# Kernel tuning notes

Measured on AMD Instinct MI355X. Metric: run time of the kernel, lower is better.

Reference implementation:

```python
import jax, jax.numpy as jnp
import numpy as np

D_MODEL = 1024
NUM_HEADS = 16
THETA = 10000.0


def _trunc_normal(key, shape):
    # matches torch.nn.init.trunc_normal_(std=std, a=-3*std, b=3*std)
    std = (2.0 / (shape[0] + shape[1])) ** 0.5
    return jax.random.truncated_normal(key, -3.0, 3.0, shape, dtype=jnp.float32) * std


def setup_inputs() -> dict:
    key = jax.random.key(0)
    kx, kq, kk, kv, ko = jax.random.split(key, 5)
    B, S, D = 2, 2048, D_MODEL
    return {
        "x": jax.random.normal(kx, (B, S, D), dtype=jnp.float32),
        "Wq": _trunc_normal(kq, (D, D)),  # torch Linear weight: [out, in]
        "Wk": _trunc_normal(kk, (D, D)),
        "Wv": _trunc_normal(kv, (D, D)),
        "Wo": _trunc_normal(ko, (D, D)),
        "token_positions": jnp.arange(S, dtype=jnp.int32),
    }


def _rope(x, token_positions):
    # x: [B, H, S, d_k]; RoPE on interleaved pairs (k r) with r=2
    d_k = x.shape[-1]
    inv_freq = THETA ** (-2.0 * jnp.arange(d_k // 2, dtype=jnp.float32) / d_k)
    ang = token_positions.astype(jnp.float32)[:, None] * inv_freq[None, :]  # [S, d_k/2]
    sin, cos = jnp.sin(ang).astype(x.dtype), jnp.cos(ang).astype(x.dtype)
    x0, x1 = x[..., 0::2], x[..., 1::2]
    y0 = x0 * cos - x1 * sin
    y1 = x0 * sin + x1 * cos
    return jnp.stack([y0, y1], axis=-1).reshape(x.shape)


def reference(x, Wq, Wk, Wv, Wo, token_positions):
    B, S, D = x.shape
    H = NUM_HEADS
    d_k = D // H

    def proj(W):  # y = x @ W^T, split heads -> [B, H, S, d_k]
        y = jnp.einsum('bsd,ed->bse', x, W)
        return y.reshape(B, S, H, d_k).transpose(0, 2, 1, 3)

    q = _rope(proj(Wq), token_positions)
    k = _rope(proj(Wk), token_positions)
    v = proj(Wv)

    # causal mask: attend where pos_k <= pos_q
    mask = token_positions[None, :] <= token_positions[:, None]  # [S_q, S_k]
    logits = jnp.einsum('bhqd,bhkd->bhqk', q, k) / (d_k ** 0.5)
    logits = jnp.where(mask, logits, -jnp.inf)
    scores = jax.nn.softmax(logits, axis=-1)
    attn = jnp.einsum('bhqk,bhkd->bhqd', scores, v)  # [B, H, S, d_k]
    attn = attn.transpose(0, 2, 1, 3).reshape(B, S, D)
    return jnp.einsum('bsd,ed->bse', attn, Wo)
```

## Files before the change

### kernel.cpp

```cpp
#include <hip/hip_runtime.h>
#include <hip/hip_bf16.h>

typedef __attribute__((ext_vector_type(8))) short s16x8;
typedef __attribute__((ext_vector_type(4))) float f32x4;

__device__ __forceinline__ unsigned short f2b(float x) {
  unsigned int u = __float_as_uint(x);
  u = (u + 0x7fffu + ((u >> 16) & 1u)) >> 16;
  return (unsigned short)u;
}

__device__ __forceinline__ unsigned int pkbf(float a, float b) {
  return (unsigned int)f2b(a) | ((unsigned int)f2b(b) << 16);
}

__device__ __forceinline__ float b2f(unsigned short u) {
  return __uint_as_float((unsigned int)u << 16);
}

__device__ __forceinline__ void gl2lds16(const unsigned short* g, unsigned short* lds) {
  __builtin_amdgcn_global_load_lds(
      (const __attribute__((address_space(1))) unsigned int*)g,
      (__attribute__((address_space(3))) unsigned int*)lds, 16, 0, 0);
}

__global__ __launch_bounds__(256) void cast_all(
    const float* __restrict__ x,  const float* __restrict__ Wq,
    const float* __restrict__ Wk, const float* __restrict__ Wv,
    const float* __restrict__ Wo, unsigned short* __restrict__ dst) {
  int i = blockIdx.x * 256 + threadIdx.x;
  const float* src;
  int off;
  if (i < 1048576) { src = x; off = i; }
  else {
    int j = i - 1048576;
    int seg = j >> 18;
    off = j & 262143;
    src = (seg == 0) ? Wq : (seg == 1) ? Wk : (seg == 2) ? Wv : Wo;
  }
  const float4 v = ((const float4*)src)[off];
  ushort4 o;
  o.x = f2b(v.x); o.y = f2b(v.y); o.z = f2b(v.z); o.w = f2b(v.w);
  ((ushort4*)dst)[i] = o;
}

#define KDIM 1024

__global__ __launch_bounds__(256, 4) void gemm_qkv(
    const unsigned short* __restrict__ A,
    const unsigned short* __restrict__ Bt,
    const int* __restrict__ tok,
    unsigned short* __restrict__ Qo,
    unsigned short* __restrict__ Ko,
    unsigned short* __restrict__ Vt) {
  __shared__ unsigned short As[2][128 * 32];
  __shared__ unsigned short Bs[2][128 * 32];
  const int tid = threadIdx.x;
  const int bid = blockIdx.x;
  const int xcd = bid & 7;
  const int loc = bid >> 3;
  const int m0 = (loc / 3) * 128;
  const int n0 = (xcd * 3 + loc % 3) * 128;
  const int w = tid >> 6, lane = tid & 63;
  const int ln = lane & 15, quad = lane >> 4;
  const int wm = (w >> 1) * 64, wn = (w & 1) * 64;

  const int rr = lane >> 2;
  const int gsw = ((lane & 3) ^ ((rr ^ (rr >> 2)) & 3)) * 8;
  const int sr = (ln ^ (ln >> 2)) & 3;

  const f32x4 zero = {0.f, 0.f, 0.f, 0.f};
  f32x4 acc[4][4];
#pragma unroll
  for (int i = 0; i < 4; ++i)
#pragma unroll
    for (int j = 0; j < 4; ++j) acc[i][j] = zero;

#define QKV_STAGE(kb, p)                                                              \
  do {                                                                                \
    int col = (kb) * 32 + gsw;                                                        \
    gl2lds16(A  + (size_t)(m0 + w * 32 + rr) * KDIM + col,      &As[p][(w * 32) * 32]);      \
    gl2lds16(A  + (size_t)(m0 + w * 32 + 16 + rr) * KDIM + col, &As[p][(w * 32 + 16) * 32]); \
    gl2lds16(Bt + (size_t)(n0 + w * 32 + rr) * KDIM + col,      &Bs[p][(w * 32) * 32]);      \
    gl2lds16(Bt + (size_t)(n0 + w * 32 + 16 + rr) * KDIM + col, &Bs[p][(w * 32 + 16) * 32]); \
  } while (0)

  QKV_STAGE(0, 0);
  for (int kb = 0; kb < 32; ++kb) {
    const int p = kb & 1;
    __syncthreads();
    if (kb < 31) QKV_STAGE(kb + 1, p ^ 1);
    s16x8 af[4], bfr[4];
#pragma unroll
    for (int i = 0; i < 4; ++i)
      af[i] = *(const s16x8*)(&As[p][(wm + i * 16 + ln) * 32 + ((quad ^ sr) * 8)]);
#pragma unroll
    for (int j = 0; j < 4; ++j)
      bfr[j] = *(const s16x8*)(&Bs[p][(wn + j * 16 + ln) * 32 + ((quad ^ sr) * 8)]);
#pragma unroll
    for (int i = 0; i < 4; ++i)
#pragma unroll
      for (int j = 0; j < 4; ++j)
        acc[i][j] = __builtin_amdgcn_mfma_f32_16x16x32_bf16(af[i], bfr[j], acc[i][j], 0, 0, 0);
  }
#undef QKV_STAGE

#pragma unroll
  for (int j = 0; j < 4; ++j) {
    int gn = n0 + wn + j * 16 + ln;
    bool isV = (gn >= 2048);
    int e = isV ? (gn - 2048) : (gn & 1023);
    int h = e >> 6, d = e & 63;
    float inv = __expf(-0.2878231366f * (float)(d >> 1));
#pragma unroll
    for (int i = 0; i < 4; ++i) {
      int gmb = m0 + wm + i * 16 + quad * 4;
#pragma unroll
      for (int r = 0; r < 4; ++r) {
        float val = acc[i][j][r];
        float part = __shfl_xor(val, 1, 64);
        int m = gmb + r;
        int b = m >> 11, s = m & 2047;
        if (!isV) {
          float pos = (float)tok[s];
          float ang = pos * inv;
          float sn, cs;
          __sincosf(ang, &sn, &cs);
          float x0 = (d & 1) ? part : val;
          float x1 = (d & 1) ? val : part;
          float y = (d & 1) ? (x0 * sn + x1 * cs) : (x0 * cs - x1 * sn);
          unsigned short* dst = (gn < 1024) ? Qo : Ko;
          dst[(((size_t)b * 16 + h) * 2048 + s) * 64 + d] = f2b(y);
        } else {
          Vt[(((size_t)b * 16 + h) * 64 + d) * 2048 + s] = f2b(val);
        }
      }
    }
  }
}

__global__ __launch_bounds__(256, 3) void attn_partial(
    const unsigned short* __restrict__ Q,
    const unsigned short* __restrict__ K,
    const unsigned short* __restrict__ Vt,
    unsigned short* __restrict__ Opart,
    float2* __restrict__ ML) {
  __shared__ unsigned short Ks[64 * 64];
  __shared__ unsigned short Vs[64 * 64];
  __shared__ unsigned short Pt[4][16 * 72];

  const int bid = blockIdx.x;
  const int xcd = bid & 7;
  const int loc = bid >> 3;
  const int bh = xcd * 4 + (loc & 3);
  const int widx = loc >> 2;
  int c, qh;
  if (widx < 28) {
    if (widx < 13)      { c = 0; qh = 3 + widx; }
    else if (widx < 22) { c = 1; qh = 7 + (widx - 13); }
    else if (widx < 27) { c = 2; qh = 11 + (widx - 22); }
    else                { c = 3; qh = 15; }
  } else {
    int s = widx - 28;
    int wt = s >> 2;
    c = s & 3;
    qh = 4 * c + 2 - wt;
  }
  const int kbeg = c * 512;
  const int khi = min(kbeg + 512, qh * 128 + 128);

  const int tid = threadIdx.x;
  const int w = tid >> 6, lane = tid & 63;
  const int ln = lane & 15, quad = lane >> 4;
  const int qb = qh * 128 + w * 32;

  const unsigned short* Qb = Q + (size_t)bh * 2048 * 64;
  const unsigned short* Kb = K + (size_t)bh * 2048 * 64;
  const unsigned short* Vb = Vt + (size_t)bh * 64 * 2048;

  const int srow = w * 16 + (lane >> 3);
  const int sg = (lane & 7) ^ (srow & 7);

  s16x8 bq[2][2];
#pragma unroll
  for (int u = 0; u < 2; ++u)
#pragma unroll
    for (int hh = 0; hh < 2; ++hh)
      bq[u][hh] = *(const s16x8*)(&Qb[(size_t)(qb + u * 16 + ln) * 64 + hh * 32 + quad * 8]);

  const f32x4 zero = {0.f, 0.f, 0.f, 0.f};
  f32x4 o[2][4];
#pragma unroll
  for (int u = 0; u < 2; ++u)
#pragma unroll
    for (int j = 0; j < 4; ++j) o[u][j] = zero;
  float m_i[2] = {-3e38f, -3e38f};
  float l_i[2] = {0.f, 0.f};

  const int rdsw = ((ln & 7) * 8);

  for (int k0 = kbeg; k0 < khi; k0 += 64) {
    __syncthreads();
    gl2lds16(Kb + (size_t)(k0 + srow) * 64 + sg * 8,       &Ks[(w * 16) * 64]);
    gl2lds16(Kb + (size_t)(k0 + srow + 8) * 64 + sg * 8,   &Ks[(w * 16 + 8) * 64]);
    gl2lds16(Vb + (size_t)srow * 2048 + k0 + sg * 8,       &Vs[(w * 16) * 64]);
    gl2lds16(Vb + (size_t)(srow + 8) * 2048 + k0 + sg * 8, &Vs[(w * 16 + 8) * 64]);
    __syncthreads();

    s16x8 ka[4][2];
#pragma unroll
    for (int t = 0; t < 4; ++t)
#pragma unroll
      for (int hh = 0; hh < 2; ++hh)
        ka[t][hh] = *(const s16x8*)(&Ks[(t * 16 + ln) * 64 + (((hh * 4 + quad) * 8) ^ rdsw)]);

#pragma unroll
    for (int u = 0; u < 2; ++u) {
      const int q = qb + u * 16 + ln;
      f32x4 st[4];
#pragma unroll
      for (int t = 0; t < 4; ++t) {
        f32x4 s = __builtin_amdgcn_mfma_f32_16x16x32_bf16(ka[t][0], bq[u][0], zero, 0, 0, 0);
        st[t] = __builtin_amdgcn_mfma_f32_16x16x32_bf16(ka[t][1], bq[u][1], s, 0, 0, 0);
      }
      float lm = -3e38f;
#pragma unroll
      for (int t = 0; t < 4; ++t)
#pragma unroll
        for (int r = 0; r < 4; ++r) {
          int kk = k0 + t * 16 + quad * 4 + r;
          float v = st[t][r] * 0.125f;
          v = (kk > q) ? -3e38f : v;
          st[t][r] = v;
          lm = fmaxf(lm, v);
        }
      lm = fmaxf(lm, __shfl_xor(lm, 16, 64));
      lm = fmaxf(lm, __shfl_xor(lm, 32, 64));
      float mn = fmaxf(m_i[u], lm);
      float al = __expf(m_i[u] - mn);
      float rs = 0.f;
#pragma unroll
      for (int t = 0; t < 4; ++t)
#pragma unroll
        for (int r = 0; r < 4; ++r) {
          float p = __expf(st[t][r] - mn);
          st[t][r] = p;
          rs += p;
        }
      rs += __shfl_xor(rs, 16, 64);
      rs += __shfl_xor(rs, 32, 64);
      m_i[u] = mn;
      l_i[u] = l_i[u] * al + rs;
#pragma unroll
      for (int j = 0; j < 4; ++j) o[u][j] *= al;

#pragma unroll
      for (int t = 0; t < 4; ++t) {
        uint2 pv;
        pv.x = pkbf(st[t][0], st[t][1]);
        pv.y = pkbf(st[t][2], st[t][3]);
        *(uint2*)(&Pt[w][ln * 72 + t * 16 + quad * 4]) = pv;
      }
      __builtin_amdgcn_wave_barrier();
#pragma unroll
      for (int hh = 0; hh < 2; ++hh) {
        s16x8 pb = *(const s16x8*)(&Pt[w][ln * 72 + hh * 32 + quad * 8]);
#pragma unroll
        for (int j = 0; j < 4; ++j) {
          s16x8 va = *(const s16x8*)(&Vs[(j * 16 + ln) * 64 + (((hh * 4 + quad) * 8) ^ rdsw)]);
          o[u][j] = __builtin_amdgcn_mfma_f32_16x16x32_bf16(va, pb, o[u][j], 0, 0, 0);
        }
      }
      __builtin_amdgcn_wave_barrier();
    }
  }

#pragma unroll
  for (int u = 0; u < 2; ++u) {
    int s = qb + u * 16 + ln;
    size_t row = ((size_t)bh * 4 + c) * 2048 + s;
    if (quad == 0) ML[row] = make_float2(m_i[u], l_i[u]);
    size_t base = row * 64;
#pragma unroll
    for (int j = 0; j < 4; ++j) {
      ushort4 o4;
      o4.x = f2b(o[u][j][0]);
      o4.y = f2b(o[u][j][1]);
      o4.z = f2b(o[u][j][2]);
      o4.w = f2b(o[u][j][3]);
      *(ushort4*)(&Opart[base + j * 16 + quad * 4]) = o4;
    }
  }
}

__global__ __launch_bounds__(256) void attn_merge(
    const unsigned short* __restrict__ Opart,
    const float2* __restrict__ ML,
    unsigned short* __restrict__ Ao) {
  int idx = blockIdx.x * 256 + threadIdx.x;
  int d0 = (idx & 7) * 8;
  int q  = (idx >> 3) & 2047;
  int bh = idx >> 14;
  int nc = (q >> 9) + 1;

  float m_c[4], l_c[4];
  float M = -3e38f;
  for (int c = 0; c < nc; ++c) {
    float2 ml = ML[((size_t)bh * 4 + c) * 2048 + q];
    m_c[c] = ml.x; l_c[c] = ml.y;
    M = fmaxf(M, ml.x);
  }
  float acc[8] = {0, 0, 0, 0, 0, 0, 0, 0};
  float L = 0.f;
  for (int c = 0; c < nc; ++c) {
    float wc = __expf(m_c[c] - M);
    L += wc * l_c[c];
    const ushort4* p = (const ushort4*)(Opart + (((size_t)bh * 4 + c) * 2048 + q) * 64 + d0);
    ushort4 a = p[0], bvec = p[1];
    acc[0] += wc * b2f(a.x); acc[1] += wc * b2f(a.y);
    acc[2] += wc * b2f(a.z); acc[3] += wc * b2f(a.w);
    acc[4] += wc * b2f(bvec.x); acc[5] += wc * b2f(bvec.y);
    acc[6] += wc * b2f(bvec.z); acc[7] += wc * b2f(bvec.w);
  }
  float invL = 1.0f / L;
  int b = bh >> 4, h = bh & 15;
  unsigned short* dst = Ao + ((size_t)b * 2048 + q) * 1024 + h * 64 + d0;
  ushort4 o0, o1;
  o0.x = f2b(acc[0] * invL); o0.y = f2b(acc[1] * invL);
  o0.z = f2b(acc[2] * invL); o0.w = f2b(acc[3] * invL);
  o1.x = f2b(acc[4] * invL); o1.y = f2b(acc[5] * invL);
  o1.z = f2b(acc[6] * invL); o1.w = f2b(acc[7] * invL);
  ((ushort4*)dst)[0] = o0;
  ((ushort4*)dst)[1] = o1;
}

__global__ __launch_bounds__(256, 3) void gemm_out(
    const unsigned short* __restrict__ A,
    const unsigned short* __restrict__ Bt,
    float* __restrict__ out) {
  __shared__ unsigned short As[2][128 * 32];
  __shared__ unsigned short Bs[2][128 * 32];
  const int tid = threadIdx.x;
  const int bid = blockIdx.x;
  const int m0 = (bid >> 3) * 128;
  const int n0 = (bid & 7) * 128;
  const int w = tid >> 6, lane = tid & 63;
  const int ln = lane & 15, quad = lane >> 4;
  const int wm = (w >> 1) * 64, wn = (w & 1) * 64;

  const int rr = lane >> 2;
  const int gsw = ((lane & 3) ^ ((rr ^ (rr >> 2)) & 3)) * 8;
  const int sr = (ln ^ (ln >> 2)) & 3;

  const f32x4 zero = {0.f, 0.f, 0.f, 0.f};
  f32x4 acc[4][4];
#pragma unroll
  for (int i = 0; i < 4; ++i)
#pragma unroll
    for (int j = 0; j < 4; ++j) acc[i][j] = zero;

#define OUT_STAGE(kb, p)                                                              \
  do {                                                                                \
    int col = (kb) * 32 + gsw;                                                        \
    gl2lds16(A  + (size_t)(m0 + w * 32 + rr) * KDIM + col,      &As[p][(w * 32) * 32]);      \
    gl2lds16(A  + (size_t)(m0 + w * 32 + 16 + rr) * KDIM + col, &As[p][(w * 32 + 16) * 32]); \
    gl2lds16(Bt + (size_t)(n0 + w * 32 + rr) * KDIM + col,      &Bs[p][(w * 32) * 32]);      \
    gl2lds16(Bt + (size_t)(n0 + w * 32 + 16 + rr) * KDIM + col, &Bs[p][(w * 32 + 16) * 32]); \
  } while (0)

  OUT_STAGE(0, 0);
  for (int kb = 0; kb < 32; ++kb) {
    const int p = kb & 1;
    __syncthreads();
    if (kb < 31) OUT_STAGE(kb + 1, p ^ 1);
    s16x8 af[4], bfr[4];
#pragma unroll
    for (int i = 0; i < 4; ++i)
      af[i] = *(const s16x8*)(&As[p][(wm + i * 16 + ln) * 32 + ((quad ^ sr) * 8)]);
#pragma unroll
    for (int j = 0; j < 4; ++j)
      bfr[j] = *(const s16x8*)(&Bs[p][(wn + j * 16 + ln) * 32 + ((quad ^ sr) * 8)]);
#pragma unroll
    for (int i = 0; i < 4; ++i)
#pragma unroll
      for (int j = 0; j < 4; ++j)
        acc[i][j] = __builtin_amdgcn_mfma_f32_16x16x32_bf16(af[i], bfr[j], acc[i][j], 0, 0, 0);
  }
#undef OUT_STAGE

#pragma unroll
  for (int i = 0; i < 4; ++i) {
    int gmb = m0 + wm + i * 16 + quad * 4;
#pragma unroll
    for (int j = 0; j < 4; ++j) {
      int gn = n0 + wn + j * 16 + ln;
#pragma unroll
      for (int r = 0; r < 4; ++r)
        out[(size_t)(gmb + r) * 1024 + gn] = acc[i][j][r];
    }
  }
}

extern "C" void kernel_launch(void* const* d_in, const int* in_sizes, int n_in,
                              void* d_out, int out_size, void* d_ws, size_t ws_size,
                              hipStream_t stream) {
  const float* x  = (const float*)d_in[0];
  const float* Wq = (const float*)d_in[1];
  const float* Wk = (const float*)d_in[2];
  const float* Wv = (const float*)d_in[3];
  const float* Wo = (const float*)d_in[4];
  const int* tok  = (const int*)d_in[5];
  float* out = (float*)d_out;

  char* ws = (char*)d_ws;
  unsigned short* xb    = (unsigned short*)(ws);
  unsigned short* Wcat  = (unsigned short*)(ws + (8ull  << 20));
  unsigned short* Wob   = (unsigned short*)(ws + (14ull << 20));
  unsigned short* Qb    = (unsigned short*)(ws + (16ull << 20));
  unsigned short* Kb    = (unsigned short*)(ws + (24ull << 20));
  unsigned short* Vtb   = (unsigned short*)(ws + (32ull << 20));
  unsigned short* Ab    = (unsigned short*)(ws + (40ull << 20));
  unsigned short* Opart = (unsigned short*)(ws + (48ull << 20));
  float2*         ML    = (float2*)        (ws + (80ull << 20));

  cast_all<<<dim3(8192), dim3(256), 0, stream>>>(x, Wq, Wk, Wv, Wo, xb);
  gemm_qkv<<<dim3(768), dim3(256), 0, stream>>>(xb, Wcat, tok, Qb, Kb, Vtb);
  attn_partial<<<dim3(1280), dim3(256), 0, stream>>>(Qb, Kb, Vtb, Opart, ML);
  attn_merge<<<dim3(2048), dim3(256), 0, stream>>>(Opart, ML, Ab);
  gemm_out<<<dim3(256), dim3(256), 0, stream>>>(Ab, Wob, out);
}
```

Before: 212.3 us.

## Double-buffer attention K/V tiles; single-buffer output GEMM with wider K tile

The attention partial kernel now double-buffers its K and V shared-memory tiles and prefetches the next 64-key tile while computing on the current one, dropping one barrier per iteration. The output projection GEMM moves the other way: it drops its double buffer for a single 128x64 buffer per operand, loads synchronously with two barriers, and uses an 8-way XOR swizzle. The GEMM change halves the number of K iterations but loses load/compute overlap. The attention change doubles K/V shared memory, which may limit occupancy.

```diff
diff --git a/kernel.cpp b/kernel.cpp
--- a/kernel.cpp
+++ b/kernel.cpp
@@ -145,8 +145,8 @@
     const unsigned short* __restrict__ Vt,
     unsigned short* __restrict__ Opart,
     float2* __restrict__ ML) {
-  __shared__ unsigned short Ks[64 * 64];
-  __shared__ unsigned short Vs[64 * 64];
+  __shared__ unsigned short Ks[2][64 * 64];
+  __shared__ unsigned short Vs[2][64 * 64];
   __shared__ unsigned short Pt[4][16 * 72];
 
   const int bid = blockIdx.x;
@@ -168,6 +168,7 @@
   }
   const int kbeg = c * 512;
   const int khi = min(kbeg + 512, qh * 128 + 128);
+  const int nit = (khi - kbeg) >> 6;
 
   const int tid = threadIdx.x;
   const int w = tid >> 6, lane = tid & 63;
@@ -181,6 +182,14 @@
   const int srow = w * 16 + (lane >> 3);
   const int sg = (lane & 7) ^ (srow & 7);
 
+#define ATTN_STAGE(k0, p)                                                            \
+  do {                                                                               \
+    gl2lds16(Kb + (size_t)((k0) + srow) * 64 + sg * 8,       &Ks[p][(w * 16) * 64]);      \
+    gl2lds16(Kb + (size_t)((k0) + srow + 8) * 64 + sg * 8,   &Ks[p][(w * 16 + 8) * 64]);  \
+    gl2lds16(Vb + (size_t)srow * 2048 + (k0) + sg * 8,       &Vs[p][(w * 16) * 64]);      \
+    gl2lds16(Vb + (size_t)(srow + 8) * 2048 + (k0) + sg * 8, &Vs[p][(w * 16 + 8) * 64]);  \
+  } while (0)
+
   s16x8 bq[2][2];
 #pragma unroll
   for (int u = 0; u < 2; ++u)
@@ -199,20 +208,19 @@
 
   const int rdsw = ((ln & 7) * 8);
 
-  for (int k0 = kbeg; k0 < khi; k0 += 64) {
+  ATTN_STAGE(kbeg, 0);
+  for (int it = 0; it < nit; ++it) {
+    const int p = it & 1;
+    const int k0 = kbeg + it * 64;
     __syncthreads();
-    gl2lds16(Kb + (size_t)(k0 + srow) * 64 + sg * 8,       &Ks[(w * 16) * 64]);
-    gl2lds16(Kb + (size_t)(k0 + srow + 8) * 64 + sg * 8,   &Ks[(w * 16 + 8) * 64]);
-    gl2lds16(Vb + (size_t)srow * 2048 + k0 + sg * 8,       &Vs[(w * 16) * 64]);
-    gl2lds16(Vb + (size_t)(srow + 8) * 2048 + k0 + sg * 8, &Vs[(w * 16 + 8) * 64]);
-    __syncthreads();
+    if (it + 1 < nit) ATTN_STAGE(k0 + 64, p ^ 1);
 
     s16x8 ka[4][2];
 #pragma unroll
     for (int t = 0; t < 4; ++t)
 #pragma unroll
       for (int hh = 0; hh < 2; ++hh)
-        ka[t][hh] = *(const s16x8*)(&Ks[(t * 16 + ln) * 64 + (((hh * 4 + quad) * 8) ^ rdsw)]);
+        ka[t][hh] = *(const s16x8*)(&Ks[p][(t * 16 + ln) * 64 + (((hh * 4 + quad) * 8) ^ rdsw)]);
 
 #pragma unroll
     for (int u = 0; u < 2; ++u) {
@@ -243,9 +251,9 @@
       for (int t = 0; t < 4; ++t)
 #pragma unroll
         for (int r = 0; r < 4; ++r) {
-          float p = __expf(st[t][r] - mn);
-          st[t][r] = p;
-          rs += p;
+          float pv = __expf(st[t][r] - mn);
+          st[t][r] = pv;
+          rs += pv;
         }
       rs += __shfl_xor(rs, 16, 64);
       rs += __shfl_xor(rs, 32, 64);
@@ -267,13 +275,14 @@
         s16x8 pb = *(const s16x8*)(&Pt[w][ln * 72 + hh * 32 + quad * 8]);
 #pragma unroll
         for (int j = 0; j < 4; ++j) {
-          s16x8 va = *(const s16x8*)(&Vs[(j * 16 + ln) * 64 + (((hh * 4 + quad) * 8) ^ rdsw)]);
+          s16x8 va = *(const s16x8*)(&Vs[p][(j * 16 + ln) * 64 + (((hh * 4 + quad) * 8) ^ rdsw)]);
           o[u][j] = __builtin_amdgcn_mfma_f32_16x16x32_bf16(va, pb, o[u][j], 0, 0, 0);
         }
       }
       __builtin_amdgcn_wave_barrier();
     }
   }
+#undef ATTN_STAGE
 
 #pragma unroll
   for (int u = 0; u < 2; ++u) {
@@ -338,8 +347,8 @@
     const unsigned short* __restrict__ A,
     const unsigned short* __restrict__ Bt,
     float* __restrict__ out) {
-  __shared__ unsigned short As[2][128 * 32];
-  __shared__ unsigned short Bs[2][128 * 32];
+  __shared__ unsigned short As[128 * 64];
+  __shared__ unsigned short Bs[128 * 64];
   const int tid = threadIdx.x;
   const int bid = blockIdx.x;
   const int m0 = (bid >> 3) * 128;
@@ -348,9 +357,9 @@
   const int ln = lane & 15, quad = lane >> 4;
   const int wm = (w >> 1) * 64, wn = (w & 1) * 64;
 
-  const int rr = lane >> 2;
-  const int gsw = ((lane & 3) ^ ((rr ^ (rr >> 2)) & 3)) * 8;
-  const int sr = (ln ^ (ln >> 2)) & 3;
+  const int srow = w * 32 + (lane >> 3);
+  const int sg = (lane & 7) ^ (lane >> 3);
+  const int rs = ln & 7;
 
   const f32x4 zero = {0.f, 0.f, 0.f, 0.f};
   f32x4 acc[4][4];
@@ -359,35 +368,30 @@
 #pragma unroll
     for (int j = 0; j < 4; ++j) acc[i][j] = zero;
 
-#define OUT_STAGE(kb, p)                                                              \
-  do {                                                                                \
-    int col = (kb) * 32 + gsw;                                                        \
-    gl2lds16(A  + (size_t)(m0 + w * 32 + rr) * KDIM + col,      &As[p][(w * 32) * 32]);      \
-    gl2lds16(A  + (size_t)(m0 + w * 32 + 16 + rr) * KDIM + col, &As[p][(w * 32 + 16) * 32]); \
-    gl2lds16(Bt + (size_t)(n0 + w * 32 + rr) * KDIM + col,      &Bs[p][(w * 32) * 32]);      \
-    gl2lds16(Bt + (size_t)(n0 + w * 32 + 16 + rr) * KDIM + col, &Bs[p][(w * 32 + 16) * 32]); \
-  } while (0)
-
-  OUT_STAGE(0, 0);
-  for (int kb = 0; kb < 32; ++kb) {
-    const int p = kb & 1;
+  for (int kb = 0; kb < KDIM / 64; ++kb) {
     __syncthreads();
-    if (kb < 31) OUT_STAGE(kb + 1, p ^ 1);
-    s16x8 af[4], bfr[4];
-#pragma unroll
-    for (int i = 0; i < 4; ++i)
-      af[i] = *(const s16x8*)(&As[p][(wm + i * 16 + ln) * 32 + ((quad ^ sr) * 8)]);
-#pragma unroll
-    for (int j = 0; j < 4; ++j)
-      bfr[j] = *(const s16x8*)(&Bs[p][(wn + j * 16 + ln) * 32 + ((quad ^ sr) * 8)]);
-#pragma unroll
-    for (int i = 0; i < 4; ++i)
+#pragma unroll
+    for (int t = 0; t < 4; ++t) {
+      gl2lds16(A  + (size_t)(m0 + srow + t * 8) * KDIM + kb * 64 + sg * 8, &As[(w * 32 + t * 8) * 64]);
+      gl2lds16(Bt + (size_t)(n0 + srow + t * 8) * KDIM + kb * 64 + sg * 8, &Bs[(w * 32 + t * 8) * 64]);
+    }
+    __syncthreads();
+#pragma unroll
+    for (int ks = 0; ks < 2; ++ks) {
+      s16x8 af[4], bfr[4];
+#pragma unroll
+      for (int i = 0; i < 4; ++i)
+        af[i] = *(const s16x8*)(&As[(wm + i * 16 + ln) * 64 + (((ks * 4 + quad) ^ rs) * 8)]);
 #pragma unroll
       for (int j = 0; j < 4; ++j)
-        acc[i][j] = __builtin_amdgcn_mfma_f32_16x16x32_bf16(af[i], bfr[j], acc[i][j], 0, 0, 0);
-  }
-#undef OUT_STAGE
-
+        bfr[j] = *(const s16x8*)(&Bs[(wn + j * 16 + ln) * 64 + (((ks * 4 + quad) ^ rs) * 8)]);
+#pragma unroll
+      for (int i = 0; i < 4; ++i)
+#pragma unroll
+        for (int j = 0; j < 4; ++j)
+          acc[i][j] = __builtin_amdgcn_mfma_f32_16x16x32_bf16(af[i], bfr[j], acc[i][j], 0, 0, 0);
+    }
+  }
 #pragma unroll
   for (int i = 0; i < 4; ++i) {
     int gmb = m0 + wm + i * 16 + quad * 4;
```

Measured after the change: 209.6 us. No clear change (-1.2%).
